# Kernel optimization log

Hardware: AMD Instinct MI355X
Metric: run time of the kernel (lower is better)

The kernel has to match this reference:

```python
import jax, jax.numpy as jnp
import numpy as np

B, T, N, E = 4, 12, 2000, 32000
ND, ED = 16, 8
H, D = 4, 16
G = H * D          # gat_hidden = 64
GH = 64            # gru_hidden
LN_EPS = 1e-5


def setup_inputs() -> dict:
    key = jax.random.key(0)
    ks = jax.random.split(key, 12)

    def xavier(k, shape):
        fan_in, fan_out = shape[0], shape[-1]
        lim = np.sqrt(6.0 / (fan_in + fan_out))
        return jax.random.uniform(k, shape, jnp.float32, -lim, lim)

    return {
        "node_features": jax.random.normal(ks[0], (B, T, N, ND), jnp.float32),
        "edge_features": jax.random.normal(ks[1], (B, T, E, ED), jnp.float32),
        "W_node": xavier(ks[2], (ND, G)),
        "W_edge": xavier(ks[3], (ED, G)),
        "att": xavier(ks[4], (H, 3 * D)),
        "ln_gamma": jnp.ones((G,), jnp.float32),
        "ln_beta": jnp.zeros((G,), jnp.float32),
        "W_ih": xavier(ks[5], (3 * GH, G)),
        "W_hh": xavier(ks[6], (3 * GH, GH)),
        "b_ih": jnp.zeros((3 * GH,), jnp.float32),
        "b_hh": jnp.zeros((3 * GH,), jnp.float32),
        "W_out": xavier(ks[7], (GH, 1)),
        "b_out": jnp.zeros((1,), jnp.float32),
        "edge_index": jax.random.randint(ks[8], (2, E), 0, N).astype(jnp.int64),
    }


def reference(node_features, edge_features, W_node, W_edge, att, ln_gamma,
              ln_beta, W_ih, W_hh, b_ih, b_hh, W_out, b_out, edge_index):
    Bv, Tv, Nv, _ = node_features.shape
    Ev = edge_features.shape[2]
    Hv = att.shape[0]
    Dv = att.shape[1] // 3
    Gv = Hv * Dv
    src, dst = edge_index[0], edge_index[1]
    a_dst, a_src, a_e = att[:, :Dv], att[:, Dv:2 * Dv], att[:, 2 * Dv:]

    def gat_single(x, ea):
        # x: [N, ND], ea: [E, ED]
        h = (x @ W_node).reshape(Nv, Hv, Dv)          # [N,H,D]
        e = (ea @ W_edge).reshape(Ev, Hv, Dv)          # [E,H,D]
        # score = LeakyReLU(a . [h_dst | h_src | e]) — compute per-node parts
        # at node level then gather (same math, avoids [E,H,3D] concat).
        s_d = jnp.einsum('nhd,hd->nh', h, a_dst)       # [N,H]
        s_s = jnp.einsum('nhd,hd->nh', h, a_src)       # [N,H]
        s_e = jnp.einsum('ehd,hd->eh', e, a_e)         # [E,H]
        score = jax.nn.leaky_relu(s_d[dst] + s_s[src] + s_e, 0.2)  # [E,H]
        # segment softmax over in-neighbours of dst
        smax = jax.ops.segment_max(score, dst, num_segments=Nv)
        exp_s = jnp.exp(score - smax[dst])
        ssum = jax.ops.segment_sum(exp_s, dst, num_segments=Nv)
        alpha = exp_s / (ssum[dst] + 1e-16)            # [E,H]
        msg = h[src] + e                               # [E,H,D]
        out = jax.ops.segment_sum(alpha[..., None] * msg, dst,
                                  num_segments=Nv)     # [N,H,D]
        out = jax.nn.elu(out).reshape(Nv, Gv)
        mu = out.mean(-1, keepdims=True)
        var = ((out - mu) ** 2).mean(-1, keepdims=True)
        out = (out - mu) / jnp.sqrt(var + LN_EPS) * ln_gamma + ln_beta
        return out, alpha

    # vmap over the B*T independent graph instances
    x_flat = node_features.reshape(Bv * Tv, Nv, -1)
    e_flat = edge_features.reshape(Bv * Tv, Ev, -1)
    gat_out, alpha_all = jax.vmap(gat_single)(x_flat, e_flat)
    spatial = gat_out.reshape(Bv, Tv, Nv, Gv)
    attn_stack = alpha_all.reshape(Bv, Tv, Ev, Hv).mean(axis=0)  # [T,E,H]

    # GRU over T (batch_first, single layer)
    gru_in = spatial.transpose(0, 2, 1, 3).reshape(Bv * Nv, Tv, Gv)
    xs = gru_in.transpose(1, 0, 2)  # [T, B*N, G]

    def gru_step(hprev, x):
        gi = x @ W_ih.T + b_ih
        gh = hprev @ W_hh.T + b_hh
        i_r, i_z, i_n = jnp.split(gi, 3, axis=-1)
        h_r, h_z, h_n = jnp.split(gh, 3, axis=-1)
        r = jax.nn.sigmoid(i_r + h_r)
        z = jax.nn.sigmoid(i_z + h_z)
        n = jnp.tanh(i_n + r * h_n)
        hnew = (1.0 - z) * n + z * hprev
        return hnew, None

    h0 = jnp.zeros((Bv * Nv, W_hh.shape[1]), gru_in.dtype)
    h_last, _ = jax.lax.scan(gru_step, h0, xs)
    h_i = h_last.reshape(Bv, Nv, -1)               # [B,N,GH]
    pred = h_i @ W_out + b_out                     # [B,N,1]
    return pred, h_i, attn_stack
```

## Files before the change

kernel.cpp:

```cpp
#include <hip/hip_runtime.h>
#include <hip/hip_bf16.h>
#include <math.h>
#include <stdint.h>

#define BQ 4
#define TQ 12
#define NQ 2000
#define EQ 32000
#define NDQ 16
#define EDQ 8
#define HQ 4
#define DQ 16
#define GQ 64
#define GHQ 64
#define NGQ 48
#define LN_EPSQ 1e-5f
#define CCAP 128

typedef _Float16 half8 __attribute__((ext_vector_type(8)));
typedef float f32x4 __attribute__((ext_vector_type(4)));

__global__ void k_count(const int* __restrict__ ei, int* __restrict__ count) {
    int e = blockIdx.x * blockDim.x + threadIdx.x;
    if (e < EQ) atomicAdd(&count[ei[EQ + e]], 1);
}

__global__ void k_scan(const int* __restrict__ count, int* __restrict__ offs,
                       int* __restrict__ cursor) {
    __shared__ int buf[2][2048];
    int t = threadIdx.x;
    for (int i = t; i < 2048; i += 1024)
        buf[0][i] = (i < NQ) ? count[i] : 0;
    __syncthreads();
    int src = 0;
    for (int sh = 1; sh < 2048; sh <<= 1) {
        int dst = src ^ 1;
        for (int i = t; i < 2048; i += 1024) {
            int v = buf[src][i];
            if (i >= sh) v += buf[src][i - sh];
            buf[dst][i] = v;
        }
        __syncthreads();
        src = dst;
    }
    for (int i = t; i <= NQ; i += 1024) {
        int off = (i == 0) ? 0 : buf[src][i - 1];
        offs[i] = off;
        if (i < NQ) cursor[i] = off;
    }
}

__global__ void k_scatter(const int* __restrict__ ei, int* __restrict__ cursor,
                          int2* __restrict__ csr2) {
    int e = blockIdx.x * blockDim.x + threadIdx.x;
    if (e < EQ) {
        int pos = atomicAdd(&cursor[ei[EQ + e]], 1);
        csr2[pos] = make_int2(e, ei[e]);
    }
}

__global__ void k_nodeproj(const float* __restrict__ xf, const float* __restrict__ Wn,
                           const float* __restrict__ att,
                           float* __restrict__ hproj, float* __restrict__ sd,
                           float* __restrict__ ss) {
    __shared__ float Wl[NDQ * GQ];
    int t = threadIdx.x;
    for (int i = t; i < NDQ * GQ; i += blockDim.x) Wl[i] = Wn[i];
    __syncthreads();
    int wid = (blockIdx.x * blockDim.x + t) >> 6;
    int lane = t & 63;
    int g = wid / NQ, n = wid % NQ;
    const float* x = xf + ((size_t)g * NQ + n) * NDQ;
    float acc = 0.f;
#pragma unroll
    for (int i = 0; i < NDQ; ++i) acc = fmaf(x[i], Wl[i * GQ + lane], acc);
    hproj[((size_t)g * NQ + n) * GQ + lane] = acc;
    int hh = lane >> 4, d = lane & 15;
    float vd = acc * att[hh * 48 + d];
    float vs = acc * att[hh * 48 + 16 + d];
#pragma unroll
    for (int s = 8; s >= 1; s >>= 1) {
        vd += __shfl_xor(vd, s, 64);
        vs += __shfl_xor(vs, s, 64);
    }
    if (d == 0) {
        sd[((size_t)g * NQ + n) * HQ + hh] = vd;
        ss[((size_t)g * NQ + n) * HQ + hh] = vs;
    }
}

__global__ void __launch_bounds__(256) k_fused(
        const float* __restrict__ ef, const float* __restrict__ We,
        const float* __restrict__ att,
        const int* __restrict__ offs, const int2* __restrict__ csr2,
        const float* __restrict__ sd, const float* __restrict__ ss,
        const float* __restrict__ hproj,
        const float* __restrict__ gamma, const float* __restrict__ beta,
        float* __restrict__ alphaG, _Float16* __restrict__ spatialH) {
    __shared__ float Wl[EDQ * GQ];
    __shared__ float WA[EDQ * HQ];
    __shared__ float ecache[4][CCAP * 4];
    __shared__ int   srcs[4][CCAP];
    __shared__ float wsum_s[4][32];
    __shared__ float hp[4][8];
    int t = threadIdx.x;
    for (int i = t; i < EDQ * GQ; i += 256) Wl[i] = We[i];
    if (t < EDQ * HQ) {
        int i = t >> 2, h4 = t & 3;
        float s = 0.f;
#pragma unroll
        for (int d = 0; d < DQ; ++d)
            s = fmaf(We[i * GQ + h4 * DQ + d], att[h4 * 48 + 32 + d], s);
        WA[t] = s;
    }
    __syncthreads();
    int w = t >> 6, lane = t & 63;
    int wid = blockIdx.x * 4 + w;
    int g = wid / NQ, n = wid % NQ;
    int beg = offs[n], deg = offs[n + 1] - beg;
    int h = lane >> 4, c = lane & 15;
    size_t ebase = (size_t)g * EQ;
    size_t nbase = (size_t)g * NQ;
    float sdv = sd[(nbase + n) * HQ + h];
    float mx = -1e30f;
    for (int k = c; k < deg; k += 16) {
        int2 pr = csr2[beg + k];
        float sse = ss[(nbase + pr.y) * HQ + h];
        const float4* ea4 = (const float4*)(ef + (ebase + pr.x) * EDQ);
        float4 lo = ea4[0], hi4 = ea4[1];
        float se = lo.x * WA[0 + h] + lo.y * WA[4 + h] + lo.z * WA[8 + h] + lo.w * WA[12 + h]
                 + hi4.x * WA[16 + h] + hi4.y * WA[20 + h] + hi4.z * WA[24 + h] + hi4.w * WA[28 + h];
        float sc = sdv + sse + se;
        sc = (sc >= 0.f) ? sc : 0.2f * sc;
        if (k < CCAP) {
            ecache[w][k * 4 + h] = sc;
            if (h == 0) srcs[w][k] = pr.y;
        }
        mx = fmaxf(mx, sc);
    }
#pragma unroll
    for (int s = 1; s < 16; s <<= 1) mx = fmaxf(mx, __shfl_xor(mx, s, 16));
    float sum = 0.f;
    float ws[8] = {0.f, 0.f, 0.f, 0.f, 0.f, 0.f, 0.f, 0.f};
    for (int k = c; k < deg; k += 16) {
        int2 pr = csr2[beg + k];
        float sc;
        if (k < CCAP) sc = ecache[w][k * 4 + h];
        else {
            float sse = ss[(nbase + pr.y) * HQ + h];
            const float4* ea4f = (const float4*)(ef + (ebase + pr.x) * EDQ);
            float4 lof = ea4f[0], hif = ea4f[1];
            float se = lof.x * WA[0 + h] + lof.y * WA[4 + h] + lof.z * WA[8 + h] + lof.w * WA[12 + h]
                     + hif.x * WA[16 + h] + hif.y * WA[20 + h] + hif.z * WA[24 + h] + hif.w * WA[28 + h];
            sc = sdv + sse + se;
            sc = (sc >= 0.f) ? sc : 0.2f * sc;
        }
        float e = __expf(sc - mx);
        if (k < CCAP) ecache[w][k * 4 + h] = e;
        sum += e;
        const float4* ea4 = (const float4*)(ef + (ebase + pr.x) * EDQ);
        float4 lo = ea4[0], hi4 = ea4[1];
        ws[0] = fmaf(e, lo.x, ws[0]); ws[1] = fmaf(e, lo.y, ws[1]);
        ws[2] = fmaf(e, lo.z, ws[2]); ws[3] = fmaf(e, lo.w, ws[3]);
        ws[4] = fmaf(e, hi4.x, ws[4]); ws[5] = fmaf(e, hi4.y, ws[5]);
        ws[6] = fmaf(e, hi4.z, ws[6]); ws[7] = fmaf(e, hi4.w, ws[7]);
    }
#pragma unroll
    for (int s = 1; s < 16; s <<= 1) sum += __shfl_xor(sum, s, 16);
    float inv = 1.f / (sum + 1e-16f);
#pragma unroll
    for (int i = 0; i < 8; ++i)
#pragma unroll
        for (int s = 1; s < 16; s <<= 1) ws[i] += __shfl_xor(ws[i], s, 16);
    if (c == 0) {
#pragma unroll
        for (int i = 0; i < 8; ++i) wsum_s[w][h * 8 + i] = ws[i] * inv;
        hp[w][h * 2] = mx; hp[w][h * 2 + 1] = inv;
    }
    for (int k = c; k < deg; k += 16) {
        int2 pr = csr2[beg + k];
        float e;
        if (k < CCAP) e = ecache[w][k * 4 + h];
        else {
            float sse = ss[(nbase + pr.y) * HQ + h];
            const float4* ea4 = (const float4*)(ef + (ebase + pr.x) * EDQ);
            float4 lo = ea4[0], hi4 = ea4[1];
            float se = lo.x * WA[0 + h] + lo.y * WA[4 + h] + lo.z * WA[8 + h] + lo.w * WA[12 + h]
                     + hi4.x * WA[16 + h] + hi4.y * WA[20 + h] + hi4.z * WA[24 + h] + hi4.w * WA[28 + h];
            float sc = sdv + sse + se;
            sc = (sc >= 0.f) ? sc : 0.2f * sc;
            e = __expf(sc - mx);
        }
        alphaG[(ebase + pr.x) * HQ + h] = e * inv;
    }
    __syncthreads();
    int dmain = deg < CCAP ? deg : CCAP;
    float acc = 0.f;
    int k = 0;
    for (; k + 4 <= dmain; k += 4) {
        float e0 = ecache[w][(k + 0) * 4 + h];
        float e1 = ecache[w][(k + 1) * 4 + h];
        float e2 = ecache[w][(k + 2) * 4 + h];
        float e3 = ecache[w][(k + 3) * 4 + h];
        int s0 = srcs[w][k + 0], s1 = srcs[w][k + 1];
        int s2 = srcs[w][k + 2], s3 = srcs[w][k + 3];
        float h0 = hproj[(nbase + s0) * GQ + lane];
        float h1 = hproj[(nbase + s1) * GQ + lane];
        float h2 = hproj[(nbase + s2) * GQ + lane];
        float h3 = hproj[(nbase + s3) * GQ + lane];
        acc = fmaf(e0, h0, acc); acc = fmaf(e1, h1, acc);
        acc = fmaf(e2, h2, acc); acc = fmaf(e3, h3, acc);
    }
    for (; k < dmain; ++k) {
        float e0 = ecache[w][k * 4 + h];
        float h0 = hproj[(nbase + srcs[w][k]) * GQ + lane];
        acc = fmaf(e0, h0, acc);
    }
    for (; k < deg; ++k) {
        int2 pr = csr2[beg + k];
        float sse = ss[(nbase + pr.y) * HQ + h];
        const float4* ea4 = (const float4*)(ef + (ebase + pr.x) * EDQ);
        float4 lo = ea4[0], hi4 = ea4[1];
        float se = lo.x * WA[0 + h] + lo.y * WA[4 + h] + lo.z * WA[8 + h] + lo.w * WA[12 + h]
                 + hi4.x * WA[16 + h] + hi4.y * WA[20 + h] + hi4.z * WA[24 + h] + hi4.w * WA[28 + h];
        float sc = sdv + sse + se;
        sc = (sc >= 0.f) ? sc : 0.2f * sc;
        float e0 = __expf(sc - hp[w][h * 2]);
        float h0 = hproj[(nbase + pr.y) * GQ + lane];
        acc = fmaf(e0, h0, acc);
    }
    acc *= hp[w][h * 2 + 1];
    float t2 = 0.f;
#pragma unroll
    for (int i = 0; i < 8; ++i) t2 = fmaf(wsum_s[w][h * 8 + i], Wl[i * GQ + lane], t2);
    float x = acc + t2;
    x = (x > 0.f) ? x : (__expf(x) - 1.f);
    float s1 = x, s2v = x * x;
#pragma unroll
    for (int s = 32; s >= 1; s >>= 1) {
        s1 += __shfl_xor(s1, s, 64);
        s2v += __shfl_xor(s2v, s, 64);
    }
    float mu = s1 * (1.f / 64.f);
    float var = s2v * (1.f / 64.f) - mu * mu;
    float y = (x - mu) * rsqrtf(var + LN_EPSQ) * gamma[lane] + beta[lane];
    spatialH[(nbase + n) * GQ + lane] = (_Float16)y;
}

__device__ inline f32x4 MF(half8 a, half8 b, f32x4 c) {
    return __builtin_amdgcn_mfma_f32_16x16x32_f16(a, b, c, 0, 0, 0);
}

__global__ void __launch_bounds__(256) k_gru(
        const _Float16* __restrict__ xh,
        const float* __restrict__ Wih, const float* __restrict__ Whh,
        const float* __restrict__ bih, const float* __restrict__ bhh,
        const float* __restrict__ Wout, const float* __restrict__ bout,
        float* __restrict__ out) {
    __shared__ _Float16 hlds[32][72];
    __shared__ float pred_s[4][32];
    int tid = threadIdx.x;
    int w = tid >> 6, l = tid & 63;
    int lr = l & 15, lg = l >> 4;
    int j = w * 16 + lr;
    half8 wiF[3][2], whF[3][2];
#pragma unroll
    for (int gb = 0; gb < 3; ++gb) {
        int q = gb * 64 + j;
#pragma unroll
        for (int kt = 0; kt < 2; ++kt) {
            const float* p  = Wih + q * 64 + kt * 32 + lg * 8;
            const float* p2 = Whh + q * 64 + kt * 32 + lg * 8;
            half8 a, b;
#pragma unroll
            for (int i = 0; i < 8; ++i) { a[i] = (_Float16)p[i]; b[i] = (_Float16)p2[i]; }
            wiF[gb][kt] = a; whF[gb][kt] = b;
        }
    }
    float br  = bih[j] + bhh[j];
    float bz  = bih[64 + j] + bhh[64 + j];
    float bin = bih[128 + j];
    float bhn = bhh[128 + j];
    float wo  = Wout[j];
    for (int i = tid; i < 32 * 72; i += 256) ((_Float16*)hlds)[i] = (_Float16)0.f;
    int id0 = blockIdx.x * 32;
    const _Float16* xp0; const _Float16* xp1;
    {
        int id = id0 + lr;          int b = id / NQ, n = id - b * NQ;
        xp0 = xh + ((size_t)b * TQ * NQ + n) * GQ + lg * 8;
        int id2 = id0 + 16 + lr;    int b2 = id2 / NQ, n2 = id2 - b2 * NQ;
        xp1 = xh + ((size_t)b2 * TQ * NQ + n2) * GQ + lg * 8;
    }
    half8 xa[2][2];
    xa[0][0] = *(const half8*)xp0; xa[0][1] = *(const half8*)(xp0 + 32);
    xa[1][0] = *(const half8*)xp1; xa[1][1] = *(const half8*)(xp1 + 32);
    float hprev[2][4] = {{0.f,0.f,0.f,0.f},{0.f,0.f,0.f,0.f}};
    __syncthreads();
    for (int t = 0; t < TQ; ++t) {
        f32x4 aR[2], aZ[2], aIN[2], aHN[2];
#pragma unroll
        for (int mt = 0; mt < 2; ++mt) {
            aR[mt]  = (f32x4){br, br, br, br};
            aZ[mt]  = (f32x4){bz, bz, bz, bz};
            aIN[mt] = (f32x4){bin, bin, bin, bin};
            aHN[mt] = (f32x4){bhn, bhn, bhn, bhn};
        }
#pragma unroll
        for (int mt = 0; mt < 2; ++mt)
#pragma unroll
            for (int kt = 0; kt < 2; ++kt) {
                aR[mt]  = MF(xa[mt][kt], wiF[0][kt], aR[mt]);
                aZ[mt]  = MF(xa[mt][kt], wiF[1][kt], aZ[mt]);
                aIN[mt] = MF(xa[mt][kt], wiF[2][kt], aIN[mt]);
            }
        half8 ha[2][2];
#pragma unroll
        for (int mt = 0; mt < 2; ++mt) {
            ha[mt][0] = *(const half8*)&hlds[16 * mt + lr][lg * 8];
            ha[mt][1] = *(const half8*)&hlds[16 * mt + lr][32 + lg * 8];
        }
#pragma unroll
        for (int mt = 0; mt < 2; ++mt)
#pragma unroll
            for (int kt = 0; kt < 2; ++kt) {
                aR[mt]  = MF(ha[mt][kt], whF[0][kt], aR[mt]);
                aZ[mt]  = MF(ha[mt][kt], whF[1][kt], aZ[mt]);
                aHN[mt] = MF(ha[mt][kt], whF[2][kt], aHN[mt]);
            }
        if (t + 1 < TQ) {
            xp0 += (size_t)NQ * GQ; xp1 += (size_t)NQ * GQ;
            xa[0][0] = *(const half8*)xp0; xa[0][1] = *(const half8*)(xp0 + 32);
            xa[1][0] = *(const half8*)xp1; xa[1][1] = *(const half8*)(xp1 + 32);
        }
#pragma unroll
        for (int mt = 0; mt < 2; ++mt)
#pragma unroll
            for (int r4 = 0; r4 < 4; ++r4) {
                float r = 1.f / (1.f + __expf(-aR[mt][r4]));
                float z = 1.f / (1.f + __expf(-aZ[mt][r4]));
                float xg = aIN[mt][r4] + r * aHN[mt][r4];
                float e2 = __expf(2.f * xg);
                float nn = 1.f - 2.f / (e2 + 1.f);
                hprev[mt][r4] = z * (hprev[mt][r4] - nn) + nn;
            }
        __syncthreads();
#pragma unroll
        for (int mt = 0; mt < 2; ++mt)
#pragma unroll
            for (int r4 = 0; r4 < 4; ++r4)
                hlds[16 * mt + 4 * lg + r4][j] = (_Float16)hprev[mt][r4];
        __syncthreads();
    }
    float pv[2][4];
#pragma unroll
    for (int mt = 0; mt < 2; ++mt)
#pragma unroll
        for (int r4 = 0; r4 < 4; ++r4) {
            int id = id0 + 16 * mt + 4 * lg + r4;
            out[8000 + (size_t)id * GHQ + j] = hprev[mt][r4];
            pv[mt][r4] = hprev[mt][r4] * wo;
        }
#pragma unroll
    for (int s = 1; s <= 8; s <<= 1)
#pragma unroll
        for (int mt = 0; mt < 2; ++mt)
#pragma unroll
            for (int r4 = 0; r4 < 4; ++r4)
                pv[mt][r4] += __shfl_xor(pv[mt][r4], s);
    if (lr == 0) {
#pragma unroll
        for (int mt = 0; mt < 2; ++mt)
#pragma unroll
            for (int r4 = 0; r4 < 4; ++r4)
                pred_s[w][16 * mt + 4 * lg + r4] = pv[mt][r4];
    }
    __syncthreads();
    if (tid < 32) {
        float s = pred_s[0][tid] + pred_s[1][tid] + pred_s[2][tid] + pred_s[3][tid] + bout[0];
        out[id0 + tid] = s;
    }
}

__global__ void k_attn(const float* __restrict__ alpha, float* __restrict__ out) {
    int gid = blockIdx.x * blockDim.x + threadIdx.x;
    if (gid >= TQ * EQ) return;
    int tt = gid / EQ, e = gid % EQ;
    float ax = 0.f, ay = 0.f, az = 0.f, aw = 0.f;
#pragma unroll
    for (int b = 0; b < BQ; ++b) {
        float4 v = *(const float4*)&alpha[(((size_t)b * TQ + tt) * EQ + e) * HQ];
        ax += v.x; ay += v.y; az += v.z; aw += v.w;
    }
    float4 r = {ax * 0.25f, ay * 0.25f, az * 0.25f, aw * 0.25f};
    *(float4*)&out[520000 + (size_t)gid * HQ] = r;
}

extern "C" void kernel_launch(void* const* d_in, const int* in_sizes, int n_in,
                              void* d_out, int out_size, void* d_ws, size_t ws_size,
                              hipStream_t stream) {
    const float* nodef = (const float*)d_in[0];
    const float* edgef = (const float*)d_in[1];
    const float* Wn    = (const float*)d_in[2];
    const float* We    = (const float*)d_in[3];
    const float* att   = (const float*)d_in[4];
    const float* gamma = (const float*)d_in[5];
    const float* beta  = (const float*)d_in[6];
    const float* Wih   = (const float*)d_in[7];
    const float* Whh   = (const float*)d_in[8];
    const float* bih   = (const float*)d_in[9];
    const float* bhh   = (const float*)d_in[10];
    const float* Wout  = (const float*)d_in[11];
    const float* bout  = (const float*)d_in[12];
    const int*   ei    = (const int*)d_in[13];

    char* ws = (char*)d_ws;
    size_t o = 0;
    int*  count  = (int*)(ws + o);  o += 2048 * 4;
    int*  offs   = (int*)(ws + o);  o += 2048 * 4;
    int*  cursor = (int*)(ws + o);  o += 2048 * 4;
    int2* csr2   = (int2*)(ws + o); o += (size_t)EQ * 8;
    float* hproj   = (float*)(ws + o); o += (size_t)NGQ * NQ * GQ * 4;
    float* sd      = (float*)(ws + o); o += (size_t)NGQ * NQ * HQ * 4;
    float* ss      = (float*)(ws + o); o += (size_t)NGQ * NQ * HQ * 4;
    float* alphaG  = (float*)(ws + o); o += (size_t)NGQ * EQ * HQ * 4;
    _Float16* spatialH = (_Float16*)(ws + o); o += (size_t)NGQ * NQ * GQ * 2;

    hipMemsetAsync(count, 0, NQ * sizeof(int), stream);
    k_count  <<<(EQ + 255) / 256, 256, 0, stream>>>(ei, count);
    k_scan   <<<1, 1024, 0, stream>>>(count, offs, cursor);
    k_scatter<<<(EQ + 255) / 256, 256, 0, stream>>>(ei, cursor, csr2);

    k_nodeproj<<<(NGQ * NQ * 64) / 256, 256, 0, stream>>>(nodef, Wn, att, hproj, sd, ss);
    k_fused   <<<(NGQ * NQ) / 4, 256, 0, stream>>>(edgef, We, att, offs, csr2,
                                                   sd, ss, hproj, gamma, beta,
                                                   alphaG, spatialH);
    k_gru     <<<(BQ * NQ) / 32, 256, 0, stream>>>(spatialH, Wih, Whh, bih, bhh,
                                                   Wout, bout, (float*)d_out);
    k_attn    <<<(TQ * EQ + 255) / 256, 256, 0, stream>>>(alphaG, (float*)d_out);
}
```

Baseline: 319.8 us.

## Store intermediates in fp16 and restructure GAT softmax passes to reuse cached edge data

Node projections and attention weights are now written and read as fp16 intermediates, which halves their global traffic. The score pass is restructured so each lane handles one edge for all four heads at once, with a single wave-wide max reduction. Edge features and edge ids are cached in shared memory, so later passes skip the repeated global gathers. The cache capacity shrinks from 128 to 64, a block-wide sync and some shared-memory staging are removed, and the extra fp16 rounding adds a small accuracy risk.

```diff
diff --git a/kernel.cpp b/kernel.cpp
--- a/kernel.cpp
+++ b/kernel.cpp
@@ -15,9 +15,10 @@
 #define GHQ 64
 #define NGQ 48
 #define LN_EPSQ 1e-5f
-#define CCAP 128
+#define CCAP 64
 
 typedef _Float16 half8 __attribute__((ext_vector_type(8)));
+typedef _Float16 half4v __attribute__((ext_vector_type(4)));
 typedef float f32x4 __attribute__((ext_vector_type(4)));
 
 __global__ void k_count(const int* __restrict__ ei, int* __restrict__ count) {
@@ -61,7 +62,7 @@
 
 __global__ void k_nodeproj(const float* __restrict__ xf, const float* __restrict__ Wn,
                            const float* __restrict__ att,
-                           float* __restrict__ hproj, float* __restrict__ sd,
+                           _Float16* __restrict__ hprojH, float* __restrict__ sd,
                            float* __restrict__ ss) {
     __shared__ float Wl[NDQ * GQ];
     int t = threadIdx.x;
@@ -74,7 +75,7 @@
     float acc = 0.f;
 #pragma unroll
     for (int i = 0; i < NDQ; ++i) acc = fmaf(x[i], Wl[i * GQ + lane], acc);
-    hproj[((size_t)g * NQ + n) * GQ + lane] = acc;
+    hprojH[((size_t)g * NQ + n) * GQ + lane] = (_Float16)acc;
     int hh = lane >> 4, d = lane & 15;
     float vd = acc * att[hh * 48 + d];
     float vs = acc * att[hh * 48 + 16 + d];
@@ -94,15 +95,15 @@
         const float* __restrict__ att,
         const int* __restrict__ offs, const int2* __restrict__ csr2,
         const float* __restrict__ sd, const float* __restrict__ ss,
-        const float* __restrict__ hproj,
+        const _Float16* __restrict__ hprojH,
         const float* __restrict__ gamma, const float* __restrict__ beta,
-        float* __restrict__ alphaG, _Float16* __restrict__ spatialH) {
+        _Float16* __restrict__ alphaH, _Float16* __restrict__ spatialH) {
     __shared__ float Wl[EDQ * GQ];
-    __shared__ float WA[EDQ * HQ];
-    __shared__ float ecache[4][CCAP * 4];
+    __shared__ __align__(16) float WA[EDQ * HQ];
+    __shared__ __align__(16) float ecache[4][CCAP * 4];
+    __shared__ half8 eac[4][CCAP];
     __shared__ int   srcs[4][CCAP];
-    __shared__ float wsum_s[4][32];
-    __shared__ float hp[4][8];
+    __shared__ int   eids[4][CCAP];
     int t = threadIdx.x;
     for (int i = t; i < EDQ * GQ; i += 256) Wl[i] = We[i];
     if (t < EDQ * HQ) {
@@ -118,82 +119,122 @@
     int wid = blockIdx.x * 4 + w;
     int g = wid / NQ, n = wid % NQ;
     int beg = offs[n], deg = offs[n + 1] - beg;
-    int h = lane >> 4, c = lane & 15;
     size_t ebase = (size_t)g * EQ;
     size_t nbase = (size_t)g * NQ;
-    float sdv = sd[(nbase + n) * HQ + h];
-    float mx = -1e30f;
-    for (int k = c; k < deg; k += 16) {
+    float4 sd4 = *(const float4*)&sd[(nbase + n) * HQ];
+    float mxr[4] = {-1e30f, -1e30f, -1e30f, -1e30f};
+    for (int k = lane; k < deg; k += 64) {
         int2 pr = csr2[beg + k];
-        float sse = ss[(nbase + pr.y) * HQ + h];
-        const float4* ea4 = (const float4*)(ef + (ebase + pr.x) * EDQ);
-        float4 lo = ea4[0], hi4 = ea4[1];
-        float se = lo.x * WA[0 + h] + lo.y * WA[4 + h] + lo.z * WA[8 + h] + lo.w * WA[12 + h]
-                 + hi4.x * WA[16 + h] + hi4.y * WA[20 + h] + hi4.z * WA[24 + h] + hi4.w * WA[28 + h];
-        float sc = sdv + sse + se;
-        sc = (sc >= 0.f) ? sc : 0.2f * sc;
+        float4 ssv = *(const float4*)&ss[(nbase + pr.y) * HQ];
+        const float4* eap = (const float4*)(ef + (ebase + pr.x) * EDQ);
+        float4 lo = eap[0], hi = eap[1];
+        float scv[4];
+#pragma unroll
+        for (int hh = 0; hh < 4; ++hh) {
+            float4 w0 = *(const float4*)&WA[0 * 4];
+            float se;
+            {
+                se =            lo.x * WA[0 * 4 + hh];
+                se = fmaf(lo.y, WA[1 * 4 + hh], se);
+                se = fmaf(lo.z, WA[2 * 4 + hh], se);
+                se = fmaf(lo.w, WA[3 * 4 + hh], se);
+                se = fmaf(hi.x, WA[4 * 4 + hh], se);
+                se = fmaf(hi.y, WA[5 * 4 + hh], se);
+                se = fmaf(hi.z, WA[6 * 4 + hh], se);
+                se = fmaf(hi.w, WA[7 * 4 + hh], se);
+            }
+            (void)w0;
+            float sdh = (hh == 0) ? sd4.x : (hh == 1) ? sd4.y : (hh == 2) ? sd4.z : sd4.w;
+            float ssh = (hh == 0) ? ssv.x : (hh == 1) ? ssv.y : (hh == 2) ? ssv.z : ssv.w;
+            float sc = sdh + ssh + se;
+            sc = (sc >= 0.f) ? sc : 0.2f * sc;
+            scv[hh] = sc;
+            mxr[hh] = fmaxf(mxr[hh], sc);
+        }
         if (k < CCAP) {
-            ecache[w][k * 4 + h] = sc;
-            if (h == 0) srcs[w][k] = pr.y;
-        }
-        mx = fmaxf(mx, sc);
-    }
-#pragma unroll
-    for (int s = 1; s < 16; s <<= 1) mx = fmaxf(mx, __shfl_xor(mx, s, 16));
+            *(float4*)&ecache[w][k * 4] = make_float4(scv[0], scv[1], scv[2], scv[3]);
+            half8 hv;
+            hv[0] = (_Float16)lo.x; hv[1] = (_Float16)lo.y;
+            hv[2] = (_Float16)lo.z; hv[3] = (_Float16)lo.w;
+            hv[4] = (_Float16)hi.x; hv[5] = (_Float16)hi.y;
+            hv[6] = (_Float16)hi.z; hv[7] = (_Float16)hi.w;
+            eac[w][k] = hv;
+            srcs[w][k] = pr.y;
+            eids[w][k] = pr.x;
+        }
+    }
+#pragma unroll
+    for (int s = 1; s < 64; s <<= 1) {
+#pragma unroll
+        for (int hh = 0; hh < 4; ++hh)
+            mxr[hh] = fmaxf(mxr[hh], __shfl_xor(mxr[hh], s, 64));
+    }
+    int h = lane >> 4, c = lane & 15;
+    float mxh = (h == 0) ? mxr[0] : (h == 1) ? mxr[1] : (h == 2) ? mxr[2] : mxr[3];
+    float sdh = (h == 0) ? sd4.x : (h == 1) ? sd4.y : (h == 2) ? sd4.z : sd4.w;
     float sum = 0.f;
     float ws[8] = {0.f, 0.f, 0.f, 0.f, 0.f, 0.f, 0.f, 0.f};
     for (int k = c; k < deg; k += 16) {
-        int2 pr = csr2[beg + k];
-        float sc;
-        if (k < CCAP) sc = ecache[w][k * 4 + h];
-        else {
-            float sse = ss[(nbase + pr.y) * HQ + h];
-            const float4* ea4f = (const float4*)(ef + (ebase + pr.x) * EDQ);
-            float4 lof = ea4f[0], hif = ea4f[1];
-            float se = lof.x * WA[0 + h] + lof.y * WA[4 + h] + lof.z * WA[8 + h] + lof.w * WA[12 + h]
-                     + hif.x * WA[16 + h] + hif.y * WA[20 + h] + hif.z * WA[24 + h] + hif.w * WA[28 + h];
-            sc = sdv + sse + se;
+        float e;
+        if (k < CCAP) {
+            e = __expf(ecache[w][k * 4 + h] - mxh);
+            ecache[w][k * 4 + h] = e;
+            half8 ev = eac[w][k];
+#pragma unroll
+            for (int i = 0; i < 8; ++i) ws[i] = fmaf(e, (float)ev[i], ws[i]);
+        } else {
+            int2 pr = csr2[beg + k];
+            float4 ssv = *(const float4*)&ss[(nbase + pr.y) * HQ];
+            float ssh = (h == 0) ? ssv.x : (h == 1) ? ssv.y : (h == 2) ? ssv.z : ssv.w;
+            const float4* eap = (const float4*)(ef + (ebase + pr.x) * EDQ);
+            float4 lo = eap[0], hi = eap[1];
+            float se =      lo.x * WA[0 * 4 + h];
+            se = fmaf(lo.y, WA[1 * 4 + h], se); se = fmaf(lo.z, WA[2 * 4 + h], se);
+            se = fmaf(lo.w, WA[3 * 4 + h], se); se = fmaf(hi.x, WA[4 * 4 + h], se);
+            se = fmaf(hi.y, WA[5 * 4 + h], se); se = fmaf(hi.z, WA[6 * 4 + h], se);
+            se = fmaf(hi.w, WA[7 * 4 + h], se);
+            float sc = sdh + ssh + se;
             sc = (sc >= 0.f) ? sc : 0.2f * sc;
-        }
-        float e = __expf(sc - mx);
-        if (k < CCAP) ecache[w][k * 4 + h] = e;
+            e = __expf(sc - mxh);
+            ws[0] = fmaf(e, lo.x, ws[0]); ws[1] = fmaf(e, lo.y, ws[1]);
+            ws[2] = fmaf(e, lo.z, ws[2]); ws[3] = fmaf(e, lo.w, ws[3]);
+            ws[4] = fmaf(e, hi.x, ws[4]); ws[5] = fmaf(e, hi.y, ws[5]);
+            ws[6] = fmaf(e, hi.z, ws[6]); ws[7] = fmaf(e, hi.w, ws[7]);
+        }
         sum += e;
-        const float4* ea4 = (const float4*)(ef + (ebase + pr.x) * EDQ);
-        float4 lo = ea4[0], hi4 = ea4[1];
-        ws[0] = fmaf(e, lo.x, ws[0]); ws[1] = fmaf(e, lo.y, ws[1]);
-        ws[2] = fmaf(e, lo.z, ws[2]); ws[3] = fmaf(e, lo.w, ws[3]);
-        ws[4] = fmaf(e, hi4.x, ws[4]); ws[5] = fmaf(e, hi4.y, ws[5]);
-        ws[6] = fmaf(e, hi4.z, ws[6]); ws[7] = fmaf(e, hi4.w, ws[7]);
-    }
-#pragma unroll
-    for (int s = 1; s < 16; s <<= 1) sum += __shfl_xor(sum, s, 16);
+    }
+#pragma unroll
+    for (int s = 1; s < 16; s <<= 1) {
+        sum += __shfl_xor(sum, s, 16);
+#pragma unroll
+        for (int i = 0; i < 8; ++i) ws[i] += __shfl_xor(ws[i], s, 16);
+    }
     float inv = 1.f / (sum + 1e-16f);
 #pragma unroll
-    for (int i = 0; i < 8; ++i)
-#pragma unroll
-        for (int s = 1; s < 16; s <<= 1) ws[i] += __shfl_xor(ws[i], s, 16);
-    if (c == 0) {
-#pragma unroll
-        for (int i = 0; i < 8; ++i) wsum_s[w][h * 8 + i] = ws[i] * inv;
-        hp[w][h * 2] = mx; hp[w][h * 2 + 1] = inv;
-    }
+    for (int i = 0; i < 8; ++i) ws[i] *= inv;
     for (int k = c; k < deg; k += 16) {
-        int2 pr = csr2[beg + k];
-        float e;
-        if (k < CCAP) e = ecache[w][k * 4 + h];
-        else {
-            float sse = ss[(nbase + pr.y) * HQ + h];
-            const float4* ea4 = (const float4*)(ef + (ebase + pr.x) * EDQ);
-            float4 lo = ea4[0], hi4 = ea4[1];
-            float se = lo.x * WA[0 + h] + lo.y * WA[4 + h] + lo.z * WA[8 + h] + lo.w * WA[12 + h]
-                     + hi4.x * WA[16 + h] + hi4.y * WA[20 + h] + hi4.z * WA[24 + h] + hi4.w * WA[28 + h];
-            float sc = sdv + sse + se;
+        float e; int eid;
+        if (k < CCAP) {
+            e = ecache[w][k * 4 + h];
+            eid = eids[w][k];
+        } else {
+            int2 pr = csr2[beg + k];
+            eid = pr.x;
+            float4 ssv = *(const float4*)&ss[(nbase + pr.y) * HQ];
+            float ssh = (h == 0) ? ssv.x : (h == 1) ? ssv.y : (h == 2) ? ssv.z : ssv.w;
+            const float4* eap = (const float4*)(ef + (ebase + pr.x) * EDQ);
+            float4 lo = eap[0], hi = eap[1];
+            float se =      lo.x * WA[0 * 4 + h];
+            se = fmaf(lo.y, WA[1 * 4 + h], se); se = fmaf(lo.z, WA[2 * 4 + h], se);
+            se = fmaf(lo.w, WA[3 * 4 + h], se); se = fmaf(hi.x, WA[4 * 4 + h], se);
+            se = fmaf(hi.y, WA[5 * 4 + h], se); se = fmaf(hi.z, WA[6 * 4 + h], se);
+            se = fmaf(hi.w, WA[7 * 4 + h], se);
+            float sc = sdh + ssh + se;
             sc = (sc >= 0.f) ? sc : 0.2f * sc;
-            e = __expf(sc - mx);
-        }
-        alphaG[(ebase + pr.x) * HQ + h] = e * inv;
-    }
-    __syncthreads();
+            e = __expf(sc - mxh);
+        }
+        alphaH[(ebase + eid) * HQ + h] = (_Float16)(e * inv);
+    }
     int dmain = deg < CCAP ? deg : CCAP;
     float acc = 0.f;
     int k = 0;
@@ -204,35 +245,39 @@
         float e3 = ecache[w][(k + 3) * 4 + h];
         int s0 = srcs[w][k + 0], s1 = srcs[w][k + 1];
         int s2 = srcs[w][k + 2], s3 = srcs[w][k + 3];
-        float h0 = hproj[(nbase + s0) * GQ + lane];
-        float h1 = hproj[(nbase + s1) * GQ + lane];
-        float h2 = hproj[(nbase + s2) * GQ + lane];
-        float h3 = hproj[(nbase + s3) * GQ + lane];
+        float h0 = (float)hprojH[(nbase + s0) * GQ + lane];
+        float h1 = (float)hprojH[(nbase + s1) * GQ + lane];
+        float h2 = (float)hprojH[(nbase + s2) * GQ + lane];
+        float h3 = (float)hprojH[(nbase + s3) * GQ + lane];
         acc = fmaf(e0, h0, acc); acc = fmaf(e1, h1, acc);
         acc = fmaf(e2, h2, acc); acc = fmaf(e3, h3, acc);
     }
     for (; k < dmain; ++k) {
         float e0 = ecache[w][k * 4 + h];
-        float h0 = hproj[(nbase + srcs[w][k]) * GQ + lane];
+        float h0 = (float)hprojH[(nbase + srcs[w][k]) * GQ + lane];
         acc = fmaf(e0, h0, acc);
     }
     for (; k < deg; ++k) {
         int2 pr = csr2[beg + k];
-        float sse = ss[(nbase + pr.y) * HQ + h];
-        const float4* ea4 = (const float4*)(ef + (ebase + pr.x) * EDQ);
-        float4 lo = ea4[0], hi4 = ea4[1];
-        float se = lo.x * WA[0 + h] + lo.y * WA[4 + h] + lo.z * WA[8 + h] + lo.w * WA[12 + h]
-                 + hi4.x * WA[16 + h] + hi4.y * WA[20 + h] + hi4.z * WA[24 + h] + hi4.w * WA[28 + h];
-        float sc = sdv + sse + se;
+        float4 ssv = *(const float4*)&ss[(nbase + pr.y) * HQ];
+        float ssh = (h == 0) ? ssv.x : (h == 1) ? ssv.y : (h == 2) ? ssv.z : ssv.w;
+        const float4* eap = (const float4*)(ef + (ebase + pr.x) * EDQ);
+        float4 lo = eap[0], hi = eap[1];
+        float se =      lo.x * WA[0 * 4 + h];
+        se = fmaf(lo.y, WA[1 * 4 + h], se); se = fmaf(lo.z, WA[2 * 4 + h], se);
+        se = fmaf(lo.w, WA[3 * 4 + h], se); se = fmaf(hi.x, WA[4 * 4 + h], se);
+        se = fmaf(hi.y, WA[5 * 4 + h], se); se = fmaf(hi.z, WA[6 * 4 + h], se);
+        se = fmaf(hi.w, WA[7 * 4 + h], se);
+        float sc = sdh + ssh + se;
         sc = (sc >= 0.f) ? sc : 0.2f * sc;
-        float e0 = __expf(sc - hp[w][h * 2]);
-        float h0 = hproj[(nbase + pr.y) * GQ + lane];
+        float e0 = __expf(sc - mxh);
+        float h0 = (float)hprojH[(nbase + pr.y) * GQ + lane];
         acc = fmaf(e0, h0, acc);
     }
-    acc *= hp[w][h * 2 + 1];
+    acc *= inv;
     float t2 = 0.f;
 #pragma unroll
-    for (int i = 0; i < 8; ++i) t2 = fmaf(wsum_s[w][h * 8 + i], Wl[i * GQ + lane], t2);
+    for (int i = 0; i < 8; ++i) t2 = fmaf(ws[i], Wl[i * GQ + lane], t2);
     float x = acc + t2;
     x = (x > 0.f) ? x : (__expf(x) - 1.f);
     float s1 = x, s2v = x * x;
@@ -381,17 +426,17 @@
     }
 }
 
-__global__ void k_attn(const float* __restrict__ alpha, float* __restrict__ out) {
+__global__ void k_attn(const _Float16* __restrict__ alpha, float* __restrict__ out) {
     int gid = blockIdx.x * blockDim.x + threadIdx.x;
     if (gid >= TQ * EQ) return;
     int tt = gid / EQ, e = gid % EQ;
-    float ax = 0.f, ay = 0.f, az = 0.f, aw = 0.f;
+    float a0 = 0.f, a1 = 0.f, a2 = 0.f, a3 = 0.f;
 #pragma unroll
     for (int b = 0; b < BQ; ++b) {
-        float4 v = *(const float4*)&alpha[(((size_t)b * TQ + tt) * EQ + e) * HQ];
-        ax += v.x; ay += v.y; az += v.z; aw += v.w;
-    }
-    float4 r = {ax * 0.25f, ay * 0.25f, az * 0.25f, aw * 0.25f};
+        half4v v = *(const half4v*)&alpha[(((size_t)b * TQ + tt) * EQ + e) * HQ];
+        a0 += (float)v[0]; a1 += (float)v[1]; a2 += (float)v[2]; a3 += (float)v[3];
+    }
+    float4 r = {a0 * 0.25f, a1 * 0.25f, a2 * 0.25f, a3 * 0.25f};
     *(float4*)&out[520000 + (size_t)gid * HQ] = r;
 }
 
@@ -419,10 +464,10 @@
     int*  offs   = (int*)(ws + o);  o += 2048 * 4;
     int*  cursor = (int*)(ws + o);  o += 2048 * 4;
     int2* csr2   = (int2*)(ws + o); o += (size_t)EQ * 8;
-    float* hproj   = (float*)(ws + o); o += (size_t)NGQ * NQ * GQ * 4;
     float* sd      = (float*)(ws + o); o += (size_t)NGQ * NQ * HQ * 4;
     float* ss      = (float*)(ws + o); o += (size_t)NGQ * NQ * HQ * 4;
-    float* alphaG  = (float*)(ws + o); o += (size_t)NGQ * EQ * HQ * 4;
+    _Float16* hprojH   = (_Float16*)(ws + o); o += (size_t)NGQ * NQ * GQ * 2;
+    _Float16* alphaH   = (_Float16*)(ws + o); o += (size_t)NGQ * EQ * HQ * 2;
     _Float16* spatialH = (_Float16*)(ws + o); o += (size_t)NGQ * NQ * GQ * 2;
 
     hipMemsetAsync(count, 0, NQ * sizeof(int), stream);
@@ -430,11 +475,11 @@
     k_scan   <<<1, 1024, 0, stream>>>(count, offs, cursor);
     k_scatter<<<(EQ + 255) / 256, 256, 0, stream>>>(ei, cursor, csr2);
 
-    k_nodeproj<<<(NGQ * NQ * 64) / 256, 256, 0, stream>>>(nodef, Wn, att, hproj, sd, ss);
+    k_nodeproj<<<(NGQ * NQ * 64) / 256, 256, 0, stream>>>(nodef, Wn, att, hprojH, sd, ss);
     k_fused   <<<(NGQ * NQ) / 4, 256, 0, stream>>>(edgef, We, att, offs, csr2,
-                                                   sd, ss, hproj, gamma, beta,
-                                                   alphaG, spatialH);
+                                                   sd, ss, hprojH, gamma, beta,
+                                                   alphaH, spatialH);
     k_gru     <<<(BQ * NQ) / 32, 256, 0, stream>>>(spatialH, Wih, Whh, bih, bhh,
                                                    Wout, bout, (float*)d_out);
-    k_attn    <<<(TQ * EQ + 255) / 256, 256, 0, stream>>>(alphaG, (float*)d_out);
-}
+    k_attn    <<<(TQ * EQ + 255) / 256, 256, 0, stream>>>(alphaH, (float*)d_out);
+}
```

Measured after the change: 297.4 us. -7.0%, faster.
